# Optimization experiments

Measured on AMD Instinct MI355X. Metric: run time of the kernel, lower is better.

## Reference

```python
import jax, jax.numpy as jnp
import numpy as np

PC_RANGE = np.array([-15.0, -30.0, -2.0, 15.0, 30.0, 2.0], np.float32)
POST_CENTER = np.array([-20.0, -35.0, -20.0, -35.0, 20.0, 35.0, 20.0, 35.0], np.float32)
MAX_NUM = 100
NUM_CLASSES = 10
SCORE_THR = 0.1

_SX = PC_RANGE[3] - PC_RANGE[0]
_SY = PC_RANGE[4] - PC_RANGE[1]


def _denorm_bbox(b):
    # cxcywh -> xyxy, then scale x coords by pc_range x-extent, y by y-extent
    cx, cy, w, h = b[..., 0], b[..., 1], b[..., 2], b[..., 3]
    xyxy = jnp.stack([cx - w / 2, cy - h / 2, cx + w / 2, cy + h / 2], axis=-1)
    scale = jnp.asarray([_SX, _SY, _SX, _SY], jnp.float32)
    off = jnp.asarray([PC_RANGE[0], PC_RANGE[1], PC_RANGE[0], PC_RANGE[1]], jnp.float32)
    return xyxy * scale + off


def _denorm_pts(p):
    scale = jnp.asarray([_SX, _SY], jnp.float32)
    off = jnp.asarray([PC_RANGE[0], PC_RANGE[1]], jnp.float32)
    return p * scale + off


def _thresh_mask(scores):
    # torch: while thresh_mask.sum()==0: tmp*=0.9; if tmp<0.01: all-true; break
    s = jax.lax.stop_gradient(scores)
    mask0 = s > SCORE_THR

    def cond(state):
        _, m = state
        return jnp.sum(m) == 0

    def body(state):
        tmp, _ = state
        tmp = tmp * 0.9
        m = jnp.where(tmp < 0.01, s > -1.0, s >= tmp)
        return (tmp, m)

    _, mask = jax.lax.while_loop(cond, body, (jnp.asarray(SCORE_THR, jnp.float32), mask0))
    return mask


def _decode_single(cls, bbox, pts):
    # cls [Q,C], bbox [Q,4], pts [Q,P,2]
    flat = jax.nn.sigmoid(cls).reshape(-1)            # [Q*C]
    scores, idx = jax.lax.top_k(flat, MAX_NUM)        # [max_num]
    labels = idx % NUM_CLASSES
    bidx = idx // NUM_CLASSES
    boxes = _denorm_bbox(bbox[bidx])                  # [max_num,4]
    p = _denorm_pts(pts[bidx])                        # [max_num,P,2]
    tmask = _thresh_mask(scores)
    rmask = jnp.all(boxes >= POST_CENTER[:4], axis=-1) & jnp.all(boxes <= POST_CENTER[4:], axis=-1)
    mask = rmask & tmask
    # fixed-size output: zero-out entries the torch code would compact away,
    # and return the boolean keep-mask.
    return (
        jnp.where(mask[:, None], boxes, 0.0),
        jnp.where(mask, scores, 0.0),
        jnp.where(mask, labels, 0),
        jnp.where(mask[:, None, None], p, 0.0),
        mask,
    )


def setup_inputs() -> dict:
    key = jax.random.key(0)
    k1, k2, k3 = jax.random.split(key, 3)
    return {
        "cls_scores": jax.random.normal(k1, (8, 100000, 10), jnp.float32),
        "bbox_preds": jax.random.uniform(k2, (8, 100000, 4), jnp.float32),
        "pts_preds": jax.random.uniform(k3, (8, 100000, 20, 2), jnp.float32),
    }


def reference(cls_scores, bbox_preds, pts_preds):
    return jax.vmap(_decode_single)(cls_scores, bbox_preds, pts_preds)
```

## Files before the change

kernel.cpp:

```cpp
#include <hip/hip_runtime.h>
#include <stdint.h>

#define B 8
#define NQ 100000
#define NCLS 10
#define NELEM 1000000
#define NV4 250000
#define KTOP 100
#define NPTS 20
#define CAP 4096
#define THREADS 256
#define CBLOCKS 128
#define REG 64
#define T0 3.6f

__device__ __forceinline__ uint32_t fkey(float x) {
  uint32_t u = __float_as_uint(x);
  return (u & 0x80000000u) ? ~u : (u | 0x80000000u);
}

__device__ __forceinline__ uint64_t composite(float logit, uint32_t idx) {
  float s = 1.0f / (1.0f + expf(-logit));
  return ((uint64_t)__float_as_uint(s) << 32) | (uint64_t)(0xFFFFFFFFu - idx);
}

__global__ void collect_kernel(const float* __restrict__ cls,
                               uint32_t* __restrict__ counts,
                               uint64_t* __restrict__ cand) {
  __shared__ uint32_t lcnt;
  int b   = blockIdx.x / CBLOCKS;
  int sub = blockIdx.x % CBLOCKS;
  if (threadIdx.x == 0) lcnt = 0;
  __syncthreads();
  const float4* src = (const float4*)(cls + (size_t)b * NELEM);
  const int STRIDE = CBLOCKS * THREADS;
  int base = sub * THREADS + threadIdx.x;
  float4 v[8];
  int   idx[8];
#pragma unroll
  for (int k = 0; k < 8; ++k) {
    idx[k] = base + k * STRIDE;
    v[k] = (idx[k] < NV4) ? src[idx[k]] : make_float4(-100.f, -100.f, -100.f, -100.f);
  }
  uint64_t* region = cand + (size_t)(b * CBLOCKS + sub) * REG;
#pragma unroll
  for (int k = 0; k < 8; ++k) {
    float xs[4] = {v[k].x, v[k].y, v[k].z, v[k].w};
#pragma unroll
    for (int l = 0; l < 4; ++l) {
      if (xs[l] > T0) {
        uint32_t slot = atomicAdd(&lcnt, 1u);
        if (slot < REG)
          region[slot] = composite(xs[l], (uint32_t)(4 * idx[k] + l));
      }
    }
  }
  __syncthreads();
  if (threadIdx.x == 0) counts[b * CBLOCKS + sub] = lcnt;
}

__global__ void final_kernel(const float* __restrict__ cls,
                             const float* __restrict__ bbox,
                             const float* __restrict__ pts,
                             const uint32_t* __restrict__ counts,
                             const uint64_t* __restrict__ cand,
                             float* __restrict__ out) {
  __shared__ uint64_t s[CAP];
  __shared__ uint32_t sc[CBLOCKS];
  __shared__ uint32_t red[THREADS];
  __shared__ uint32_t s_bad, s_cnt;
  int b = blockIdx.x;
  int tid = threadIdx.x;

  if (tid == 0) { s_bad = 0; }
  __syncthreads();

  uint32_t myc = 0;
  if (tid < CBLOCKS) {
    myc = counts[b * CBLOCKS + tid];
    if (myc > REG) { s_bad = 1; myc = REG; }
    sc[tid] = myc;
  }
  for (int step = 1; step < CBLOCKS; step <<= 1) {
    __syncthreads();
    uint32_t add = (tid < CBLOCKS && tid >= step) ? sc[tid - step] : 0;
    __syncthreads();
    if (tid < CBLOCKS) sc[tid] += add;
  }
  __syncthreads();
  uint32_t total = sc[CBLOCKS - 1];
  uint32_t bad = s_bad || (total < KTOP) || (total > CAP);
  __syncthreads();

  uint32_t cnt;
  if (!bad) {
    if (tid < CBLOCKS) {
      uint32_t off = sc[tid] - myc;
      const uint64_t* region = cand + (size_t)(b * CBLOCKS + tid) * REG;
      for (uint32_t j = 0; j < myc; ++j) s[off + j] = region[j];
    }
    cnt = total;
  } else {
    const float* src = cls + (size_t)b * NELEM;
    uint32_t lo = 0, hi = 0xFFFFFFFFu;
    while (lo < hi) {
      uint32_t mid = lo + ((hi - lo + 1) >> 1);
      uint32_t c = 0;
      for (int i = tid; i < NELEM; i += THREADS)
        c += (fkey(src[i]) >= mid) ? 1u : 0u;
      red[tid] = c;
      __syncthreads();
      for (int off = THREADS / 2; off > 0; off >>= 1) {
        if (tid < off) red[tid] += red[tid + off];
        __syncthreads();
      }
      uint32_t totc = red[0];
      __syncthreads();
      if (totc >= KTOP) lo = mid; else hi = mid - 1;
    }
    uint32_t T = lo;
    if (tid == 0) s_cnt = 0;
    __syncthreads();
    for (int i = tid; i < NELEM; i += THREADS) {
      float x = src[i];
      if (fkey(x) > T) {
        uint32_t slot = atomicAdd(&s_cnt, 1u);
        s[slot] = composite(x, (uint32_t)i);
      }
    }
    __syncthreads();
    if (tid == 0) {
      uint32_t nGT = s_cnt, got = 0;
      for (int i = 0; i < NELEM && nGT + got < KTOP; ++i) {
        float x = src[i];
        if (fkey(x) == T) { s[nGT + got] = composite(x, (uint32_t)i); got++; }
      }
      s_cnt = KTOP;
    }
    __syncthreads();
    cnt = s_cnt;
  }

  uint32_t n = 256;
  while (n < cnt) n <<= 1;
  for (uint32_t i = cnt + tid; i < n; i += THREADS) s[i] = 0ull;
  __syncthreads();

  for (uint32_t k = 2; k <= n; k <<= 1) {
    for (uint32_t j = k >> 1; j > 0; j >>= 1) {
      for (uint32_t i = tid; i < n; i += THREADS) {
        uint32_t ixj = i ^ j;
        if (ixj > i) {
          uint64_t a = s[i], c = s[ixj];
          bool desc = ((i & k) == 0);
          if (desc ? (a < c) : (a > c)) { s[i] = c; s[ixj] = a; }
        }
      }
      __syncthreads();
    }
  }

  float smax = __uint_as_float((uint32_t)(s[0] >> 32));
  int mode;
  float thr = 0.1f;
  if (smax > 0.1f) {
    mode = 0;
  } else {
    float tmp = 0.1f;
    mode = 2;
    while (true) {
      tmp *= 0.9f;
      if (tmp < 0.01f) { mode = 2; break; }
      if (smax >= tmp) { mode = 1; thr = tmp; break; }
    }
  }
  if (tid < KTOP) {
    uint64_t comp = s[tid];
    float score = __uint_as_float((uint32_t)(comp >> 32));
    uint32_t idx = 0xFFFFFFFFu - (uint32_t)(comp & 0xFFFFFFFFu);
    uint32_t label = idx % NCLS;
    uint32_t bidx = idx / NCLS;
    if (bidx >= NQ) bidx = 0;
    float4 bb = ((const float4*)(bbox + (size_t)b * NQ * 4))[bidx];
    float hx = __fmul_rn(bb.z, 0.5f);
    float hy = __fmul_rn(bb.w, 0.5f);
    float x1 = __fadd_rn(__fmul_rn(__fsub_rn(bb.x, hx), 30.0f), -15.0f);
    float y1 = __fadd_rn(__fmul_rn(__fsub_rn(bb.y, hy), 60.0f), -30.0f);
    float x2 = __fadd_rn(__fmul_rn(__fadd_rn(bb.x, hx), 30.0f), -15.0f);
    float y2 = __fadd_rn(__fmul_rn(__fadd_rn(bb.y, hy), 60.0f), -30.0f);
    bool rmask = (x1 >= -20.0f) & (y1 >= -35.0f) & (x2 >= -20.0f) & (y2 >= -35.0f) &
                 (x1 <= 20.0f) & (y1 <= 35.0f) & (x2 <= 20.0f) & (y2 <= 35.0f);
    bool tmask = (mode == 2) || (mode == 0 ? (score > thr) : (score >= thr));
    bool mask = rmask && tmask;

    float* oBoxes  = out;
    float* oScores = out + B * KTOP * 4;
    float* oLabels = oScores + B * KTOP;
    float* oPts    = oLabels + B * KTOP;
    float* oMask   = oPts + B * KTOP * NPTS * 2;
    size_t rb = (size_t)b * KTOP + (size_t)tid;

    ((float4*)oBoxes)[rb] = mask ? make_float4(x1, y1, x2, y2)
                                 : make_float4(0.f, 0.f, 0.f, 0.f);
    oScores[rb] = mask ? score : 0.0f;
    oLabels[rb] = mask ? (float)label : 0.0f;
    oMask[rb]   = mask ? 1.0f : 0.0f;

    const float4* ps = (const float4*)(pts + (size_t)b * NQ * NPTS * 2 + (size_t)bidx * NPTS * 2);
    float4* po = (float4*)(oPts + rb * NPTS * 2);
#pragma unroll
    for (int j = 0; j < 10; ++j) {
      float4 p = ps[j];
      float4 o;
      o.x = __fadd_rn(__fmul_rn(p.x, 30.0f), -15.0f);
      o.y = __fadd_rn(__fmul_rn(p.y, 60.0f), -30.0f);
      o.z = __fadd_rn(__fmul_rn(p.z, 30.0f), -15.0f);
      o.w = __fadd_rn(__fmul_rn(p.w, 60.0f), -30.0f);
      po[j] = mask ? o : make_float4(0.f, 0.f, 0.f, 0.f);
    }
  }
}

extern "C" void kernel_launch(void* const* d_in, const int* in_sizes, int n_in,
                              void* d_out, int out_size, void* d_ws, size_t ws_size,
                              hipStream_t stream) {
  const float* cls  = (const float*)d_in[0];
  const float* bbox = (const float*)d_in[1];
  const float* pts  = (const float*)d_in[2];
  float* out = (float*)d_out;

  uint8_t* ws = (uint8_t*)d_ws;
  uint32_t* counts = (uint32_t*)ws;
  uint64_t* cand   = (uint64_t*)(ws + B * CBLOCKS * 4);

  collect_kernel<<<B * CBLOCKS, THREADS, 0, stream>>>(cls, counts, cand);
  final_kernel<<<B, THREADS, 0, stream>>>(cls, bbox, pts, counts, cand, out);
}
```

Before: 190.4 us.

## Fuse collect and final kernels via last-block-done atomic counter

Merges the candidate-collection kernel and the per-batch top-k finalization kernel into one launch. The last block to finish for each batch, detected with an atomic counter, does the merge, sort and output. This removes one kernel launch and its gap, at the cost of a memset launch for the counters. The shared sort buffer shrinks from 4096 to 1024 entries so the fused kernel can keep occupancy in the collection phase, but any batch with more than 1024 candidates now takes the slow exact-threshold fallback path.

After: 316.0 us. 1.66x slower.

```diff
diff --git a/kernel.cpp b/kernel.cpp
--- a/kernel.cpp
+++ b/kernel.cpp
@@ -8,7 +8,7 @@
 #define NV4 250000
 #define KTOP 100
 #define NPTS 20
-#define CAP 4096
+#define CAP 1024
 #define THREADS 256
 #define CBLOCKS 128
 #define REG 64
@@ -24,55 +24,59 @@
   return ((uint64_t)__float_as_uint(s) << 32) | (uint64_t)(0xFFFFFFFFu - idx);
 }
 
-__global__ void collect_kernel(const float* __restrict__ cls,
-                               uint32_t* __restrict__ counts,
-                               uint64_t* __restrict__ cand) {
-  __shared__ uint32_t lcnt;
-  int b   = blockIdx.x / CBLOCKS;
-  int sub = blockIdx.x % CBLOCKS;
-  if (threadIdx.x == 0) lcnt = 0;
-  __syncthreads();
-  const float4* src = (const float4*)(cls + (size_t)b * NELEM);
-  const int STRIDE = CBLOCKS * THREADS;
-  int base = sub * THREADS + threadIdx.x;
-  float4 v[8];
-  int   idx[8];
-#pragma unroll
-  for (int k = 0; k < 8; ++k) {
-    idx[k] = base + k * STRIDE;
-    v[k] = (idx[k] < NV4) ? src[idx[k]] : make_float4(-100.f, -100.f, -100.f, -100.f);
-  }
-  uint64_t* region = cand + (size_t)(b * CBLOCKS + sub) * REG;
-#pragma unroll
-  for (int k = 0; k < 8; ++k) {
-    float xs[4] = {v[k].x, v[k].y, v[k].z, v[k].w};
-#pragma unroll
-    for (int l = 0; l < 4; ++l) {
-      if (xs[l] > T0) {
-        uint32_t slot = atomicAdd(&lcnt, 1u);
-        if (slot < REG)
-          region[slot] = composite(xs[l], (uint32_t)(4 * idx[k] + l));
-      }
-    }
-  }
-  __syncthreads();
-  if (threadIdx.x == 0) counts[b * CBLOCKS + sub] = lcnt;
-}
-
-__global__ void final_kernel(const float* __restrict__ cls,
+__global__ void fused_kernel(const float* __restrict__ cls,
                              const float* __restrict__ bbox,
                              const float* __restrict__ pts,
-                             const uint32_t* __restrict__ counts,
-                             const uint64_t* __restrict__ cand,
+                             uint32_t* __restrict__ counts,
+                             uint64_t* __restrict__ cand,
+                             uint32_t* __restrict__ done,
                              float* __restrict__ out) {
   __shared__ uint64_t s[CAP];
   __shared__ uint32_t sc[CBLOCKS];
   __shared__ uint32_t red[THREADS];
-  __shared__ uint32_t s_bad, s_cnt;
-  int b = blockIdx.x;
+  __shared__ uint32_t lcnt, s_old, s_bad, s_cnt;
+
+  int b   = blockIdx.x / CBLOCKS;
+  int sub = blockIdx.x % CBLOCKS;
   int tid = threadIdx.x;
 
-  if (tid == 0) { s_bad = 0; }
+  if (tid == 0) lcnt = 0;
+  __syncthreads();
+  {
+    const float4* src = (const float4*)(cls + (size_t)b * NELEM);
+    const int STRIDE = CBLOCKS * THREADS;
+    int base = sub * THREADS + tid;
+    float4 v[8];
+    int   idx[8];
+#pragma unroll
+    for (int k = 0; k < 8; ++k) {
+      idx[k] = base + k * STRIDE;
+      v[k] = (idx[k] < NV4) ? src[idx[k]] : make_float4(-100.f, -100.f, -100.f, -100.f);
+    }
+    uint64_t* region = cand + (size_t)(b * CBLOCKS + sub) * REG;
+#pragma unroll
+    for (int k = 0; k < 8; ++k) {
+      float xs[4] = {v[k].x, v[k].y, v[k].z, v[k].w};
+#pragma unroll
+      for (int l = 0; l < 4; ++l) {
+        if (xs[l] > T0) {
+          uint32_t slot = atomicAdd(&lcnt, 1u);
+          if (slot < REG)
+            region[slot] = composite(xs[l], (uint32_t)(4 * idx[k] + l));
+        }
+      }
+    }
+  }
+  __syncthreads();
+  if (tid == 0) counts[b * CBLOCKS + sub] = lcnt;
+
+  __threadfence();
+  if (tid == 0) s_old = atomicAdd(&done[b], 1u);
+  __syncthreads();
+  if (s_old != CBLOCKS - 1) return;
+  __threadfence();
+
+  if (tid == 0) s_bad = 0;
   __syncthreads();
 
   uint32_t myc = 0;
@@ -231,8 +235,9 @@
 
   uint8_t* ws = (uint8_t*)d_ws;
   uint32_t* counts = (uint32_t*)ws;
-  uint64_t* cand   = (uint64_t*)(ws + B * CBLOCKS * 4);
-
-  collect_kernel<<<B * CBLOCKS, THREADS, 0, stream>>>(cls, counts, cand);
-  final_kernel<<<B, THREADS, 0, stream>>>(cls, bbox, pts, counts, cand, out);
-}
+  uint32_t* done   = (uint32_t*)(ws + B * CBLOCKS * 4);
+  uint64_t* cand   = (uint64_t*)(ws + B * CBLOCKS * 4 + 256);
+
+  hipMemsetAsync(done, 0, B * sizeof(uint32_t), stream);
+  fused_kernel<<<B * CBLOCKS, THREADS, 0, stream>>>(cls, bbox, pts, counts, cand, done, out);
+}
```
